# Kernel tuning notes

Measured on AMD Instinct MI355X. Metric: run time of the kernel, lower is better.

The kernel has to match this reference:

```python
import jax, jax.numpy as jnp
import numpy as np

B, S, H = 4, 1024, 1024
NH, HD = 16, 64          # heads, head_dim (NH*HD == H)
E, K, I = 8, 2, 1024     # routed experts, top_k, expert intermediate
NSH = 2                  # shared experts -> shared intermediate = NSH*I
EPS = 1e-6


def setup_inputs() -> dict:
    key = jax.random.key(0)
    ks = jax.random.split(key, 12)
    init = lambda k, shape: (jax.random.normal(k, shape, jnp.float32) * 0.02)
    return {
        "hidden_states": jax.random.normal(ks[0], (B, S, H), jnp.float32),
        "conditioning": jax.random.normal(ks[1], (B, H), jnp.float32),
        "adaLN_W": init(ks[2], (H, 6 * H)),
        "ln1_scale": jnp.ones((H,), jnp.float32),
        "ln1_bias": jnp.zeros((H,), jnp.float32),
        "ln2_scale": jnp.ones((H,), jnp.float32),
        "ln2_bias": jnp.zeros((H,), jnp.float32),
        "Wq": init(ks[3], (H, H)),
        "Wk": init(ks[4], (H, H)),
        "Wv": init(ks[5], (H, H)),
        "Wo": init(ks[6], (H, H)),
        "gate_kernel": init(ks[7], (E, H)),
        "We1": init(ks[8], (E, H, I)),
        "We2": init(ks[9], (E, I, H)),
        "Ws1": init(ks[10], (H, NSH * I)),
        "Ws2": init(ks[11], (NSH * I, H)),
    }


def _layernorm(x, scale, bias):
    m = x.mean(-1, keepdims=True)
    v = x.var(-1, keepdims=True)
    return (x - m) * jax.lax.rsqrt(v + EPS) * scale + bias


def _modulate(x, shift, scale):
    # (1 + scale) * x + shift, broadcasting [B,H] conditioning over seq dim
    return x * (1.0 + scale[:, None, :]) + shift[:, None, :]


def _attention(x, Wq, Wk, Wv, Wo):
    b, s, h = x.shape
    q = (x @ Wq).reshape(b, s, NH, HD)
    k = (x @ Wk).reshape(b, s, NH, HD)
    v = (x @ Wv).reshape(b, s, NH, HD)
    scores = jnp.einsum("bqnd,bknd->bnqk", q, k) / np.sqrt(HD).astype(np.float32)
    probs = jax.nn.softmax(scores, axis=-1)
    out = jnp.einsum("bnqk,bknd->bqnd", probs, v).reshape(b, s, h)
    return out @ Wo


def reference(hidden_states, conditioning, adaLN_W, ln1_scale, ln1_bias,
              ln2_scale, ln2_bias, Wq, Wk, Wv, Wo, gate_kernel, We1, We2,
              Ws1, Ws2):
    # adaLN modulation: SiLU -> Linear(H, 6H) -> chunk 6
    mods = jax.nn.silu(conditioning) @ adaLN_W  # [B, 6H]
    (shift_msa, scale_msa, gate_msa,
     shift_mlp, scale_mlp, gate_mlp) = jnp.split(mods, 6, axis=-1)

    normed = _modulate(_layernorm(hidden_states, ln1_scale, ln1_bias),
                       shift_msa, scale_msa)
    attn_out = _attention(normed, Wq, Wk, Wv, Wo)
    h = hidden_states + gate_msa[:, None, :] * attn_out

    normed2 = _modulate(_layernorm(h, ln2_scale, ln2_bias),
                        shift_mlp, scale_mlp)

    # --- MoE gate (DeepSeek-V2 style, greedy top-k, softmax scoring) ---
    logits = jnp.einsum("bsh,eh->bse", normed2.astype(jnp.float32),
                        gate_kernel.astype(jnp.float32))
    scores = jax.nn.softmax(logits, axis=-1)           # [B,S,E]
    topk_w, topk_idx = jax.lax.top_k(scores, K)        # [B,S,K]
    topk_w = topk_w / (topk_w.sum(-1, keepdims=True) + 1e-20)  # norm_topk_prob

    # --- dense all-expert MLPs then top-k combine (as in DiTMLPMoE) ---
    eh = jax.nn.gelu(jnp.einsum("bsh,ehi->ebsi", normed2, We1))  # [E,B,S,I]
    eo = jnp.einsum("ebsi,eih->bseh", eh, We2)                   # [B,S,E,H]
    sel = jnp.take_along_axis(eo, topk_idx[..., None], axis=2)   # [B,S,K,H]
    y = (sel * topk_w[..., None].astype(sel.dtype)).sum(axis=2)  # [B,S,H]

    # shared experts (always active)
    y = y + jax.nn.gelu(normed2 @ Ws1) @ Ws2

    return h + gate_mlp[:, None, :] * y
```

## Files before the change

### kernel.cpp

```cpp
#include <hip/hip_runtime.h>

typedef __bf16 bf16x8 __attribute__((ext_vector_type(8)));
typedef __bf16 bf16x4 __attribute__((ext_vector_type(4)));
typedef float  f32x4  __attribute__((ext_vector_type(4)));

__device__ inline float wred_sum(float v){
  #pragma unroll
  for (int d = 1; d < 64; d <<= 1) v += __shfl_xor(v, d, 64);
  return v;
}

__device__ inline float gelu_t(float x){
  const float c0 = 0.7978845608028654f;
  float t = tanhf(c0 * (x + 0.044715f * x * x * x));
  return 0.5f * x * (1.0f + t);
}

__device__ __forceinline__ void gload_lds16(const __bf16* g, __bf16* l){
  __builtin_amdgcn_global_load_lds((const __attribute__((address_space(1))) void*)g,
                                   (__attribute__((address_space(3))) void*)l, 16, 0, 0);
}

__global__ __launch_bounds__(256)
void transpose_all(const float* __restrict__ Wq, const float* __restrict__ Wk,
                   const float* __restrict__ Wv, const float* __restrict__ Wo,
                   const float* __restrict__ Ws1, const float* __restrict__ Ws2,
                   const float* __restrict__ We1, const float* __restrict__ We2,
                   __bf16* __restrict__ qkvT, __bf16* __restrict__ WoT,
                   __bf16* __restrict__ Ws1T, __bf16* __restrict__ Ws2T,
                   __bf16* __restrict__ We1T, __bf16* __restrict__ We2T){
  int z = blockIdx.z;
  const float* src; long ss; __bf16* dst; long ds;
  const long M1 = 1024 * 1024;
  if (z < 3)      { src = (z == 0 ? Wq : z == 1 ? Wk : Wv); ss = 1024; dst = qkvT + (long)z * M1; ds = 1024; }
  else if (z == 3){ src = Wo; ss = 1024; dst = WoT; ds = 1024; }
  else if (z < 6) { int ch = z - 4; src = Ws1 + ch * 1024; ss = 2048; dst = Ws1T + (long)ch * M1; ds = 1024; }
  else if (z < 8) { int rh = z - 6; src = Ws2 + (long)rh * M1; ss = 1024; dst = Ws2T + rh * 1024; ds = 2048; }
  else if (z < 16){ int e = z - 8;  src = We1 + (long)e * M1; ss = 1024; dst = We1T + (long)e * M1; ds = 1024; }
  else            { int e = z - 16; src = We2 + (long)e * M1; ss = 1024; dst = We2T + (long)e * M1; ds = 1024; }
  __shared__ float t[32][33];
  int r0 = blockIdx.y * 32, c0 = blockIdx.x * 32;
  int tid = threadIdx.x;
  int tr = tid >> 3, tc = (tid & 7) * 4;
  float4 vv = *(const float4*)&src[(long)(r0 + tr) * ss + c0 + tc];
  t[tr][tc + 0] = vv.x; t[tr][tc + 1] = vv.y; t[tr][tc + 2] = vv.z; t[tr][tc + 3] = vv.w;
  __syncthreads();
  int oc = tid >> 3, orr = (tid & 7) * 4;
  bf16x4 o4;
  #pragma unroll
  for (int i = 0; i < 4; i++) o4[i] = (__bf16)t[orr + i][oc];
  *(bf16x4*)&dst[(long)(c0 + oc) * ds + r0 + orr] = o4;
}

__global__ __launch_bounds__(256)
void adaln_k(const float* __restrict__ cond, const float* __restrict__ W, float* __restrict__ mods){
  int col = blockIdx.x * 256 + threadIdx.x;
  int kc  = blockIdx.y;
  __shared__ float sc[4][256];
  for (int i = threadIdx.x; i < 1024; i += 256){
    int b = i >> 8, r = i & 255;
    float x = cond[b * 1024 + kc * 256 + r];
    sc[b][r] = x / (1.f + expf(-x));
  }
  __syncthreads();
  float a0 = 0.f, a1 = 0.f, a2 = 0.f, a3 = 0.f;
  #pragma unroll 4
  for (int i = 0; i < 256; i++){
    float wv = W[(long)(kc * 256 + i) * 6144 + col];
    a0 += sc[0][i] * wv; a1 += sc[1][i] * wv;
    a2 += sc[2][i] * wv; a3 += sc[3][i] * wv;
  }
  atomicAdd(&mods[0 * 6144 + col], a0);
  atomicAdd(&mods[1 * 6144 + col], a1);
  atomicAdd(&mods[2 * 6144 + col], a2);
  atomicAdd(&mods[3 * 6144 + col], a3);
}

__global__ __launch_bounds__(256)
void ln_mod(const float* __restrict__ x, const float* __restrict__ sc, const float* __restrict__ bi,
            const float* __restrict__ mods, int shift_off, int scale_off, __bf16* __restrict__ out){
  int row = blockIdx.x, tid = threadIdx.x, b = row >> 10;
  float4 xv = *(const float4*)&x[(long)row * 1024 + tid * 4];
  float s  = xv.x + xv.y + xv.z + xv.w;
  float s2 = xv.x * xv.x + xv.y * xv.y + xv.z * xv.z + xv.w * xv.w;
  s = wred_sum(s); s2 = wred_sum(s2);
  __shared__ float ssum[4], ssum2[4];
  int w = tid >> 6;
  if ((tid & 63) == 0){ ssum[w] = s; ssum2[w] = s2; }
  __syncthreads();
  s = ssum[0] + ssum[1] + ssum[2] + ssum[3];
  s2 = ssum2[0] + ssum2[1] + ssum2[2] + ssum2[3];
  float mean = s * (1.f / 1024.f);
  float var  = s2 * (1.f / 1024.f) - mean * mean;
  float inv  = rsqrtf(var + 1e-6f);
  const float xa[4] = {xv.x, xv.y, xv.z, xv.w};
  #pragma unroll
  for (int i = 0; i < 4; i++){
    int c = tid * 4 + i;
    float nv = (xa[i] - mean) * inv * sc[c] + bi[c];
    nv = nv * (1.f + mods[b * 6144 + scale_off + c]) + mods[b * 6144 + shift_off + c];
    out[(long)row * 1024 + c] = (__bf16)nv;
  }
}

__global__ __launch_bounds__(256)
void gate_k(const float* __restrict__ h, const float* __restrict__ ln2s, const float* __restrict__ ln2b,
            const float* __restrict__ mods, const float* __restrict__ gw,
            int* __restrict__ eidx, float* __restrict__ wpair, __bf16* __restrict__ n2o){
  __shared__ float gws[8192];
  int tid = threadIdx.x;
  #pragma unroll
  for (int i = 0; i < 8; i++){
    int idx = tid + i * 256;
    *(float4*)&gws[idx * 4] = *(const float4*)&gw[idx * 4];
  }
  __syncthreads();
  int wv = tid >> 6, lane = tid & 63;
  int tok = blockIdx.x * 4 + wv;
  int b = tok >> 10;
  float4 xv[4]; float s = 0.f, s2 = 0.f;
  #pragma unroll
  for (int ch = 0; ch < 4; ch++){
    float4 v = *(const float4*)&h[(long)tok * 1024 + ch * 256 + lane * 4];
    xv[ch] = v;
    s  += v.x + v.y + v.z + v.w;
    s2 += v.x * v.x + v.y * v.y + v.z * v.z + v.w * v.w;
  }
  s = wred_sum(s); s2 = wred_sum(s2);
  float mean = s * (1.f / 1024.f);
  float var  = s2 * (1.f / 1024.f) - mean * mean;
  float inv  = rsqrtf(var + 1e-6f);
  float lg[8];
  #pragma unroll
  for (int e = 0; e < 8; e++) lg[e] = 0.f;
  #pragma unroll
  for (int ch = 0; ch < 4; ch++){
    int c = ch * 256 + lane * 4;
    float4 s4  = *(const float4*)&ln2s[c];
    float4 b4  = *(const float4*)&ln2b[c];
    float4 sc4 = *(const float4*)&mods[b * 6144 + 4096 + c];
    float4 sh4 = *(const float4*)&mods[b * 6144 + 3072 + c];
    float v0 = ((xv[ch].x - mean) * inv * s4.x + b4.x) * (1.f + sc4.x) + sh4.x;
    float v1 = ((xv[ch].y - mean) * inv * s4.y + b4.y) * (1.f + sc4.y) + sh4.y;
    float v2 = ((xv[ch].z - mean) * inv * s4.z + b4.z) * (1.f + sc4.z) + sh4.z;
    float v3 = ((xv[ch].w - mean) * inv * s4.w + b4.w) * (1.f + sc4.w) + sh4.w;
    *(bf16x4*)&n2o[(long)tok * 1024 + c] = (bf16x4){(__bf16)v0, (__bf16)v1, (__bf16)v2, (__bf16)v3};
    #pragma unroll
    for (int e = 0; e < 8; e++){
      float4 g4 = *(const float4*)&gws[e * 1024 + c];
      lg[e] += v0 * g4.x + v1 * g4.y + v2 * g4.z + v3 * g4.w;
    }
  }
  #pragma unroll
  for (int e = 0; e < 8; e++) lg[e] = wred_sum(lg[e]);
  if (lane == 0){
    float mx = lg[0];
    #pragma unroll
    for (int e = 1; e < 8; e++) mx = fmaxf(mx, lg[e]);
    float p[8], ss = 0.f;
    #pragma unroll
    for (int e = 0; e < 8; e++){ p[e] = expf(lg[e] - mx); ss += p[e]; }
    #pragma unroll
    for (int e = 0; e < 8; e++) p[e] /= ss;
    int i0 = 0; float b0 = p[0];
    #pragma unroll
    for (int e = 1; e < 8; e++) if (p[e] > b0){ b0 = p[e]; i0 = e; }
    int i1 = -1; float b1 = -1.f;
    #pragma unroll
    for (int e = 0; e < 8; e++) if (e != i0 && p[e] > b1){ b1 = p[e]; i1 = e; }
    float dn = b0 + b1 + 1e-20f;
    eidx[tok * 2]     = i0; wpair[tok * 2]     = b0 / dn;
    eidx[tok * 2 + 1] = i1; wpair[tok * 2 + 1] = b1 / dn;
  }
}

__global__ __launch_bounds__(256)
void build_k(const int* __restrict__ eidx, int* __restrict__ counts, int* __restrict__ lists){
  int e = blockIdx.x;
  int tid = threadIdx.x, wv = tid >> 6, lane = tid & 63;
  __shared__ int base;
  __shared__ int woff[4];
  if (tid == 0) base = 0;
  __syncthreads();
  for (int it = 0; it < 32; ++it){
    int i = it * 256 + tid;
    bool m = (eidx[i] == e);
    unsigned long long bal = __ballot(m);
    int prefix = __popcll(bal & ((1ull << lane) - 1ull));
    if (lane == 0) woff[wv] = __popcll(bal);
    __syncthreads();
    int off = base;
    #pragma unroll
    for (int k = 0; k < 4; k++) if (k < wv) off += woff[k];
    if (m) lists[e * 4096 + off + prefix] = i;
    __syncthreads();
    if (tid == 0) base += woff[0] + woff[1] + woff[2] + woff[3];
    __syncthreads();
  }
  if (tid == 0) counts[e] = base;
}

__global__ __launch_bounds__(256)
void attn_k(const __bf16* __restrict__ qkv, __bf16* __restrict__ og){
  int p = blockIdx.x + blockIdx.y * 8;
  int qblk = (p >> 3) & 7;
  int bh   = (p & 7) + ((p >> 6) << 3);
  int bb = bh >> 4, hn = bh & 15;
  int q0 = qblk * 128;
  long tokbase = (long)bb * 1024;
  int hd0 = hn * 64;
  int tid = threadIdx.x; int w = tid >> 6; int lane = tid & 63;

  __shared__ __bf16 Ks[64][76];
  __shared__ __bf16 Vt[64][76];
  __shared__ __bf16 Ps[4][32][76];

  const float QS = 0.125f * 1.44269504088896f;
  bf16x8 qf[2][2];
  #pragma unroll
  for (int sub = 0; sub < 2; sub++){
    long qrow = tokbase + q0 + sub * 64 + w * 16 + (lane & 15);
    qf[sub][0] = *(const bf16x8*)&qkv[qrow * 3072 + hd0 + (lane >> 4) * 8];
    qf[sub][1] = *(const bf16x8*)&qkv[qrow * 3072 + hd0 + 32 + (lane >> 4) * 8];
    #pragma unroll
    for (int i = 0; i < 8; i++){
      qf[sub][0][i] = (__bf16)((float)qf[sub][0][i] * QS);
      qf[sub][1][i] = (__bf16)((float)qf[sub][1][i] * QS);
    }
  }

  __bf16 one_b = (__bf16)1.0f;
  bf16x8 one8 = (bf16x8){one_b, one_b, one_b, one_b, one_b, one_b, one_b, one_b};

  float m_r[2][4];
  f32x4 oa[2][4];
  f32x4 lacc[2];
  #pragma unroll
  for (int sub = 0; sub < 2; sub++){
    lacc[sub] = (f32x4){0.f, 0.f, 0.f, 0.f};
    #pragma unroll
    for (int r = 0; r < 4; r++) m_r[sub][r] = -1e30f;
    #pragma unroll
    for (int hb = 0; hb < 4; hb++) oa[sub][hb] = (f32x4){0.f, 0.f, 0.f, 0.f};
  }

  int dcol = tid & 63, rblk = tid >> 6;
  for (int t = 0; t < 16; t++){
    long kvbase = tokbase + t * 64;
    #pragma unroll
    for (int pp = 0; pp < 2; pp++){
      int r = (tid >> 3) + pp * 32;
      int c = (tid & 7) * 8;
      *(bf16x8*)&Ks[r][c] = *(const bf16x8*)&qkv[(kvbase + r) * 3072 + 1024 + hd0 + c];
    }
    bf16x8 col0, col1;
    #pragma unroll
    for (int i = 0; i < 8; i++)
      col0[i] = qkv[(kvbase + rblk * 16 + i) * 3072 + 2048 + hd0 + dcol];
    #pragma unroll
    for (int i = 0; i < 8; i++)
      col1[i] = qkv[(kvbase + rblk * 16 + 8 + i) * 3072 + 2048 + hd0 + dcol];
    *(bf16x8*)&Vt[dcol][rblk * 16]     = col0;
    *(bf16x8*)&Vt[dcol][rblk * 16 + 8] = col1;
    __syncthreads();

    #pragma unroll
    for (int sub = 0; sub < 2; sub++){
      f32x4 sf[4];
      #pragma unroll
      for (int cb = 0; cb < 4; cb++){
        bf16x8 kf0 = *(const bf16x8*)&Ks[cb * 16 + (lane & 15)][(lane >> 4) * 8];
        bf16x8 kf1 = *(const bf16x8*)&Ks[cb * 16 + (lane & 15)][32 + (lane >> 4) * 8];
        f32x4 sacc = (f32x4){0.f, 0.f, 0.f, 0.f};
        sacc = __builtin_amdgcn_mfma_f32_16x16x32_bf16(qf[sub][0], kf0, sacc, 0, 0, 0);
        sacc = __builtin_amdgcn_mfma_f32_16x16x32_bf16(qf[sub][1], kf1, sacc, 0, 0, 0);
        sf[cb] = sacc;
      }
      float mxr[4]; float dmax = -1e30f;
      #pragma unroll
      for (int r = 0; r < 4; r++){
        float mx = fmaxf(fmaxf(sf[0][r], sf[1][r]), fmaxf(sf[2][r], sf[3][r]));
        #pragma unroll
        for (int d = 1; d < 16; d <<= 1) mx = fmaxf(mx, __shfl_xor(mx, d, 64));
        mxr[r] = mx;
        dmax = fmaxf(dmax, mx - m_r[sub][r]);
      }
      if (!__all(dmax <= 8.f)){
        #pragma unroll
        for (int r = 0; r < 4; r++){
          float mn = fmaxf(m_r[sub][r], mxr[r]);
          float fr = __builtin_amdgcn_exp2f(m_r[sub][r] - mn);
          m_r[sub][r] = mn;
          lacc[sub][r] *= fr;
          #pragma unroll
          for (int hb = 0; hb < 4; hb++) oa[sub][hb][r] *= fr;
        }
      }
      #pragma unroll
      for (int cb = 0; cb < 4; cb++)
        #pragma unroll
        for (int r = 0; r < 4; r++)
          Ps[w][sub * 16 + (lane >> 4) * 4 + r][cb * 16 + (lane & 15)] =
            (__bf16)__builtin_amdgcn_exp2f(sf[cb][r] - m_r[sub][r]);
    }
    bf16x8 pf[2][2];
    #pragma unroll
    for (int sub = 0; sub < 2; sub++){
      pf[sub][0] = *(const bf16x8*)&Ps[w][sub * 16 + (lane & 15)][(lane >> 4) * 8];
      pf[sub][1] = *(const bf16x8*)&Ps[w][sub * 16 + (lane & 15)][32 + (lane >> 4) * 8];
      lacc[sub] = __builtin_amdgcn_mfma_f32_16x16x32_bf16(pf[sub][0], one8, lacc[sub], 0, 0, 0);
      lacc[sub] = __builtin_amdgcn_mfma_f32_16x16x32_bf16(pf[sub][1], one8, lacc[sub], 0, 0, 0);
    }
    #pragma unroll
    for (int hb = 0; hb < 4; hb++){
      bf16x8 vf0 = *(const bf16x8*)&Vt[hb * 16 + (lane & 15)][(lane >> 4) * 8];
      bf16x8 vf1 = *(const bf16x8*)&Vt[hb * 16 + (lane & 15)][32 + (lane >> 4) * 8];
      #pragma unroll
      for (int sub = 0; sub < 2; sub++){
        oa[sub][hb] = __builtin_amdgcn_mfma_f32_16x16x32_bf16(pf[sub][0], vf0, oa[sub][hb], 0, 0, 0);
        oa[sub][hb] = __builtin_amdgcn_mfma_f32_16x16x32_bf16(pf[sub][1], vf1, oa[sub][hb], 0, 0, 0);
      }
    }
    __syncthreads();
  }
  #pragma unroll
  for (int sub = 0; sub < 2; sub++)
    #pragma unroll
    for (int hb = 0; hb < 4; hb++)
      #pragma unroll
      for (int r = 0; r < 4; r++){
        long row = tokbase + q0 + sub * 64 + w * 16 + (lane >> 4) * 4 + r;
        float val = oa[sub][hb][r] / lacc[sub][r];
        og[row * 1024 + hd0 + hb * 16 + (lane & 15)] = (__bf16)val;
      }
}

template<int EPI, int GMODE>
__global__ __launch_bounds__(256)
void gemm_k(const __bf16* __restrict__ A, int lda,
            const __bf16* __restrict__ Bt, int K, long bstride,
            const int* __restrict__ lists, const int* __restrict__ counts,
            __bf16* __restrict__ outb, int ldo,
            float* __restrict__ outf,
            const float* __restrict__ resid,
            const float* __restrict__ mods, int mod_off,
            const float* __restrict__ wpair,
            const float* __restrict__ addin){
  int e = blockIdx.z;
  int cnt = 1 << 30;
  const int* list = nullptr;
  if (GMODE){
    cnt = counts[e];
    if ((int)blockIdx.y * 128 >= cnt) return;
    list = lists + e * 4096;
    Bt += (long)e * bstride;
  }
  int row0 = blockIdx.y * 128;
  int n0 = blockIdx.x * 128;
  int tid = threadIdx.x;
  int lane = tid & 63, w = tid >> 6;
  int wr = (w >> 1) * 64, wc = (w & 1) * 64;

  __shared__ __bf16 As[2 * 128 * 64];
  __shared__ __bf16 Bs[2 * 128 * 64];

  f32x4 acc[4][4];
  #pragma unroll
  for (int m = 0; m < 4; m++)
    #pragma unroll
    for (int n = 0; n < 4; n++) acc[m][n] = (f32x4){0.f, 0.f, 0.f, 0.f};

  long aoff[4]; const __bf16* bptr[4];
  #pragma unroll
  for (int j = 0; j < 4; j++){
    int r = w * 32 + j * 8 + (lane >> 3);
    int scb = (lane & 7) ^ (r & 7);
    int gr = row0 + r;
    int srcr;
    if (GMODE == 0) srcr = gr;
    else if (gr < cnt){ int pv = list[gr]; srcr = (GMODE == 1) ? (pv >> 1) : pv; }
    else { int pv = list[0]; srcr = (GMODE == 1) ? (pv >> 1) : pv; }
    aoff[j] = (long)srcr * lda + scb * 8;
    bptr[j] = Bt + (long)(n0 + r) * K + scb * 8;
  }
  const int nk = K / 64;
  #pragma unroll
  for (int j = 0; j < 4; j++){
    gload_lds16(A + aoff[j], &As[(w * 32 + j * 8) * 64]);
    gload_lds16(bptr[j],     &Bs[(w * 32 + j * 8) * 64]);
  }
  __syncthreads();
  int cur = 0;
  for (int kt = 0; kt < nk; ++kt){
    int nxt = cur ^ 1;
    if (kt + 1 < nk){
      int k0 = (kt + 1) * 64;
      #pragma unroll
      for (int j = 0; j < 4; j++){
        gload_lds16(A + aoff[j] + k0, &As[nxt * 8192 + (w * 32 + j * 8) * 64]);
        gload_lds16(bptr[j] + k0,     &Bs[nxt * 8192 + (w * 32 + j * 8) * 64]);
      }
    }
    #pragma unroll
    for (int ks = 0; ks < 2; ++ks){
      bf16x8 af[4], bfr[4];
      #pragma unroll
      for (int m = 0; m < 4; m++){
        int r = wr + m * 16 + (lane & 15);
        int blk = (ks * 4 + (lane >> 4)) ^ (r & 7);
        af[m] = *(const bf16x8*)&As[cur * 8192 + r * 64 + blk * 8];
      }
      #pragma unroll
      for (int n = 0; n < 4; n++){
        int r = wc + n * 16 + (lane & 15);
        int blk = (ks * 4 + (lane >> 4)) ^ (r & 7);
        bfr[n] = *(const bf16x8*)&Bs[cur * 8192 + r * 64 + blk * 8];
      }
      #pragma unroll
      for (int m = 0; m < 4; m++)
        #pragma unroll
        for (int n = 0; n < 4; n++)
          acc[m][n] = __builtin_amdgcn_mfma_f32_16x16x32_bf16(af[m], bfr[n], acc[m][n], 0, 0, 0);
    }
    __syncthreads();
    cur = nxt;
  }
  #pragma unroll
  for (int m = 0; m < 4; m++){
    #pragma unroll
    for (int r = 0; r < 4; r++){
      int rl = wr + m * 16 + (lane >> 4) * 4 + r;
      int grow = row0 + rl;
      if (GMODE && grow >= cnt) continue;
      #pragma unroll
      for (int n = 0; n < 4; n++){
        int col = n0 + wc + n * 16 + (lane & 15);
        float v = acc[m][n][r];
        if (EPI == 0){
          outb[(long)grow * ldo + col] = (__bf16)v;
        } else if (EPI == 1){
          int dst = (GMODE == 1) ? list[grow] : grow;
          outb[(long)dst * ldo + col] = (__bf16)gelu_t(v);
        } else if (EPI == 2){
          int b = grow >> 10;
          outf[(long)grow * 1024 + col] = resid[(long)grow * 1024 + col] + mods[b * 6144 + mod_off + col] * v;
        } else if (EPI == 4){
          int pv = list[grow];
          atomicAdd(&outf[(long)(pv >> 1) * 1024 + col], wpair[pv] * v);
        } else if (EPI == 5){
          int b = grow >> 10;
          outf[(long)grow * 1024 + col] = resid[(long)grow * 1024 + col]
              + mods[b * 6144 + mod_off + col] * (v + addin[(long)grow * 1024 + col]);
        }
      }
    }
  }
}

extern "C" void kernel_launch(void* const* d_in, const int* in_sizes, int n_in,
                              void* d_out, int out_size, void* d_ws, size_t ws_size,
                              hipStream_t stream){
  const float* hidden = (const float*)d_in[0];
  const float* cond   = (const float*)d_in[1];
  const float* adaW   = (const float*)d_in[2];
  const float* ln1s   = (const float*)d_in[3];
  const float* ln1b   = (const float*)d_in[4];
  const float* ln2s   = (const float*)d_in[5];
  const float* ln2b   = (const float*)d_in[6];
  const float* Wq     = (const float*)d_in[7];
  const float* Wk     = (const float*)d_in[8];
  const float* Wv     = (const float*)d_in[9];
  const float* Wo     = (const float*)d_in[10];
  const float* gatek  = (const float*)d_in[11];
  const float* We1    = (const float*)d_in[12];
  const float* We2    = (const float*)d_in[13];
  const float* Ws1    = (const float*)d_in[14];
  const float* Ws2    = (const float*)d_in[15];
  float* out = (float*)d_out;

  const size_t MB = 1024 * 1024;
  char* W = (char*)d_ws;
  size_t off = 0;
  auto take = [&](size_t b) -> void* {
    void* p = W + off;
    off += (b + 255) & ~((size_t)255);
    return p;
  };
  float*  mods   = (float*) take(4 * 6144 * sizeof(float));
  float*  yb     = (float*) take(16 * MB);
  __bf16* qkvT   = (__bf16*)take(6 * MB);
  __bf16* WoT    = (__bf16*)take(2 * MB);
  __bf16* Ws1T   = (__bf16*)take(4 * MB);
  __bf16* Ws2T   = (__bf16*)take(4 * MB);
  __bf16* We1T   = (__bf16*)take(16 * MB);
  __bf16* We2T   = (__bf16*)take(16 * MB);
  __bf16* n1     = (__bf16*)take(8 * MB);
  __bf16* ab     = (__bf16*)take(8 * MB);
  __bf16* qkv    = (__bf16*)take(24 * MB);
  float*  hb     = (float*) take(16 * MB);
  __bf16* n2     = (__bf16*)take(8 * MB);
  int*    counts = (int*)   take(256);
  int*    lists  = (int*)   take(8 * 4096 * 4);
  float*  wpair  = (float*) take(8192 * 4);
  int*    eidx   = (int*)   take(8192 * 4);
  __bf16* EH = n1;
  __bf16* SH = qkv;

  dim3 blk(256);

  hipMemsetAsync(mods, 0, 4 * 6144 * sizeof(float) + 16 * MB, stream);

  transpose_all<<<dim3(32, 32, 24), blk, 0, stream>>>(Wq, Wk, Wv, Wo, Ws1, Ws2, We1, We2,
                                                      qkvT, WoT, Ws1T, Ws2T, We1T, We2T);

  adaln_k<<<dim3(24, 4), blk, 0, stream>>>(cond, adaW, mods);

  ln_mod<<<4096, blk, 0, stream>>>(hidden, ln1s, ln1b, mods, 0, 1024, n1);

  gemm_k<0, 0><<<dim3(24, 32, 1), blk, 0, stream>>>(n1, 1024, qkvT, 1024, 0, nullptr, nullptr, qkv, 3072, nullptr, nullptr, nullptr, 0, nullptr, nullptr);

  attn_k<<<dim3(8, 64, 1), blk, 0, stream>>>(qkv, ab);

  gemm_k<2, 0><<<dim3(8, 32, 1), blk, 0, stream>>>(ab, 1024, WoT, 1024, 0, nullptr, nullptr, nullptr, 0, hb, hidden, mods, 2048, nullptr, nullptr);

  gate_k<<<1024, blk, 0, stream>>>(hb, ln2s, ln2b, mods, gatek, eidx, wpair, n2);
  build_k<<<8, blk, 0, stream>>>(eidx, counts, lists);

  gemm_k<1, 1><<<dim3(8, 32, 8), blk, 0, stream>>>(n2, 1024, We1T, 1024, 1048576, lists, counts, EH, 1024, nullptr, nullptr, nullptr, 0, nullptr, nullptr);
  gemm_k<4, 2><<<dim3(8, 32, 8), blk, 0, stream>>>(EH, 1024, We2T, 1024, 1048576, lists, counts, nullptr, 0, yb, nullptr, nullptr, 0, wpair, nullptr);

  gemm_k<1, 0><<<dim3(16, 32, 1), blk, 0, stream>>>(n2, 1024, Ws1T, 1024, 0, nullptr, nullptr, SH, 2048, nullptr, nullptr, nullptr, 0, nullptr, nullptr);
  gemm_k<5, 0><<<dim3(8, 32, 1), blk, 0, stream>>>(SH, 2048, Ws2T, 2048, 0, nullptr, nullptr, nullptr, 0, out, hb, mods, 5120, nullptr, yb);

  (void)in_sizes; (void)n_in; (void)out_size; (void)ws_size;
}
```

Baseline: 560.9 us.

## Merge routed and shared up-projection GEMMs, replace atomics with bf16 scatter buffer

The GEMM kernel moves to 512 threads with 8 waves each holding a 64x32 sub-tile, and drops the LDS double buffering in favour of a single-stage load-then-compute loop. The routed expert up-projection and the shared-expert up-projection now run in one launch, selected by the z index. The down-projection writes weighted per-pair outputs to a bf16 buffer instead of doing float atomicAdds, and the final shared GEMM epilogue sums the two pair rows. This removes the atomics, the 16 MB memset and one launch, at the cost of losing load/compute overlap inside the GEMM and rounding the expert outputs to bf16.

```diff
diff --git a/kernel.cpp b/kernel.cpp
--- a/kernel.cpp
+++ b/kernel.cpp
@@ -336,94 +336,101 @@
 }
 
 template<int EPI, int GMODE>
-__global__ __launch_bounds__(256)
+__global__ __launch_bounds__(512)
 void gemm_k(const __bf16* __restrict__ A, int lda,
             const __bf16* __restrict__ Bt, int K, long bstride,
+            const __bf16* __restrict__ Bt2,
             const int* __restrict__ lists, const int* __restrict__ counts,
             __bf16* __restrict__ outb, int ldo,
+            __bf16* __restrict__ outb2, int ldo2,
             float* __restrict__ outf,
             const float* __restrict__ resid,
             const float* __restrict__ mods, int mod_off,
             const float* __restrict__ wpair,
-            const float* __restrict__ addin){
-  int e = blockIdx.z;
+            const __bf16* __restrict__ eo){
+  int z = blockIdx.z;
   int cnt = 1 << 30;
   const int* list = nullptr;
-  if (GMODE){
-    cnt = counts[e];
+  const __bf16* B = Bt;
+  __bf16* OB = outb; int LDO = ldo;
+  bool shp = false;
+  if (GMODE == 2){
+    cnt = counts[z];
     if ((int)blockIdx.y * 128 >= cnt) return;
-    list = lists + e * 4096;
-    Bt += (long)e * bstride;
+    list = lists + z * 4096;
+    B = Bt + (long)z * bstride;
+  } else if (GMODE == 3){
+    if (z < 8){
+      cnt = counts[z];
+      if ((int)blockIdx.y * 128 >= cnt) return;
+      list = lists + z * 4096;
+      B = Bt + (long)z * bstride;
+    } else {
+      shp = true;
+      B = Bt2 + (long)(z - 8) * bstride;
+      OB = outb2 + (long)(z - 8) * 1024; LDO = ldo2;
+    }
   }
   int row0 = blockIdx.y * 128;
   int n0 = blockIdx.x * 128;
   int tid = threadIdx.x;
   int lane = tid & 63, w = tid >> 6;
-  int wr = (w >> 1) * 64, wc = (w & 1) * 64;
-
-  __shared__ __bf16 As[2 * 128 * 64];
-  __shared__ __bf16 Bs[2 * 128 * 64];
-
-  f32x4 acc[4][4];
+  int wr = (w >> 2) * 64, wc = (w & 3) * 32;
+
+  __shared__ __bf16 As[128 * 64];
+  __shared__ __bf16 Bs[128 * 64];
+
+  f32x4 acc[4][2];
   #pragma unroll
   for (int m = 0; m < 4; m++)
     #pragma unroll
-    for (int n = 0; n < 4; n++) acc[m][n] = (f32x4){0.f, 0.f, 0.f, 0.f};
-
-  long aoff[4]; const __bf16* bptr[4];
-  #pragma unroll
-  for (int j = 0; j < 4; j++){
-    int r = w * 32 + j * 8 + (lane >> 3);
+    for (int n = 0; n < 2; n++) acc[m][n] = (f32x4){0.f, 0.f, 0.f, 0.f};
+
+  long aoff[2]; const __bf16* bptr[2];
+  #pragma unroll
+  for (int j = 0; j < 2; j++){
+    int r = j * 64 + w * 8 + (lane >> 3);
     int scb = (lane & 7) ^ (r & 7);
     int gr = row0 + r;
     int srcr;
-    if (GMODE == 0) srcr = gr;
-    else if (gr < cnt){ int pv = list[gr]; srcr = (GMODE == 1) ? (pv >> 1) : pv; }
-    else { int pv = list[0]; srcr = (GMODE == 1) ? (pv >> 1) : pv; }
+    bool routed = (GMODE == 2) || (GMODE == 3 && !shp);
+    if (!routed) srcr = gr;
+    else if (gr < cnt){ int pv = list[gr]; srcr = (GMODE == 3) ? (pv >> 1) : pv; }
+    else { int pv = list[0]; srcr = (GMODE == 3) ? (pv >> 1) : pv; }
     aoff[j] = (long)srcr * lda + scb * 8;
-    bptr[j] = Bt + (long)(n0 + r) * K + scb * 8;
+    bptr[j] = B + (long)(n0 + r) * K + scb * 8;
   }
   const int nk = K / 64;
-  #pragma unroll
-  for (int j = 0; j < 4; j++){
-    gload_lds16(A + aoff[j], &As[(w * 32 + j * 8) * 64]);
-    gload_lds16(bptr[j],     &Bs[(w * 32 + j * 8) * 64]);
-  }
-  __syncthreads();
-  int cur = 0;
   for (int kt = 0; kt < nk; ++kt){
-    int nxt = cur ^ 1;
-    if (kt + 1 < nk){
-      int k0 = (kt + 1) * 64;
-      #pragma unroll
-      for (int j = 0; j < 4; j++){
-        gload_lds16(A + aoff[j] + k0, &As[nxt * 8192 + (w * 32 + j * 8) * 64]);
-        gload_lds16(bptr[j] + k0,     &Bs[nxt * 8192 + (w * 32 + j * 8) * 64]);
-      }
-    }
+    int k0 = kt * 64;
+    #pragma unroll
+    for (int j = 0; j < 2; j++){
+      gload_lds16(A + aoff[j] + k0, &As[(j * 64 + w * 8) * 64]);
+      gload_lds16(bptr[j] + k0,     &Bs[(j * 64 + w * 8) * 64]);
+    }
+    __syncthreads();
     #pragma unroll
     for (int ks = 0; ks < 2; ++ks){
-      bf16x8 af[4], bfr[4];
+      bf16x8 af[4], bfr[2];
       #pragma unroll
       for (int m = 0; m < 4; m++){
         int r = wr + m * 16 + (lane & 15);
         int blk = (ks * 4 + (lane >> 4)) ^ (r & 7);
-        af[m] = *(const bf16x8*)&As[cur * 8192 + r * 64 + blk * 8];
-      }
-      #pragma unroll
-      for (int n = 0; n < 4; n++){
+        af[m] = *(const bf16x8*)&As[r * 64 + blk * 8];
+      }
+      #pragma unroll
+      for (int n = 0; n < 2; n++){
         int r = wc + n * 16 + (lane & 15);
         int blk = (ks * 4 + (lane >> 4)) ^ (r & 7);
-        bfr[n] = *(const bf16x8*)&Bs[cur * 8192 + r * 64 + blk * 8];
+        bfr[n] = *(const bf16x8*)&Bs[r * 64 + blk * 8];
       }
       #pragma unroll
       for (int m = 0; m < 4; m++)
         #pragma unroll
-        for (int n = 0; n < 4; n++)
+        for (int n = 0; n < 2; n++)
           acc[m][n] = __builtin_amdgcn_mfma_f32_16x16x32_bf16(af[m], bfr[n], acc[m][n], 0, 0, 0);
     }
     __syncthreads();
-    cur = nxt;
   }
   #pragma unroll
   for (int m = 0; m < 4; m++){
@@ -431,26 +438,27 @@
     for (int r = 0; r < 4; r++){
       int rl = wr + m * 16 + (lane >> 4) * 4 + r;
       int grow = row0 + rl;
-      if (GMODE && grow >= cnt) continue;
-      #pragma unroll
-      for (int n = 0; n < 4; n++){
+      if ((GMODE == 2 || (GMODE == 3 && !shp)) && grow >= cnt) continue;
+      #pragma unroll
+      for (int n = 0; n < 2; n++){
         int col = n0 + wc + n * 16 + (lane & 15);
         float v = acc[m][n][r];
         if (EPI == 0){
-          outb[(long)grow * ldo + col] = (__bf16)v;
+          OB[(long)grow * LDO + col] = (__bf16)v;
         } else if (EPI == 1){
-          int dst = (GMODE == 1) ? list[grow] : grow;
-          outb[(long)dst * ldo + col] = (__bf16)gelu_t(v);
+          int dst = (GMODE == 3 && !shp) ? list[grow] : grow;
+          OB[(long)dst * LDO + col] = (__bf16)gelu_t(v);
         } else if (EPI == 2){
           int b = grow >> 10;
           outf[(long)grow * 1024 + col] = resid[(long)grow * 1024 + col] + mods[b * 6144 + mod_off + col] * v;
-        } else if (EPI == 4){
-          int pv = list[grow];
-          atomicAdd(&outf[(long)(pv >> 1) * 1024 + col], wpair[pv] * v);
         } else if (EPI == 5){
           int b = grow >> 10;
+          float add = (float)eo[(long)(grow * 2) * 1024 + col] + (float)eo[(long)(grow * 2 + 1) * 1024 + col];
           outf[(long)grow * 1024 + col] = resid[(long)grow * 1024 + col]
-              + mods[b * 6144 + mod_off + col] * (v + addin[(long)grow * 1024 + col]);
+              + mods[b * 6144 + mod_off + col] * (v + add);
+        } else if (EPI == 6){
+          int pv = list[grow];
+          OB[(long)pv * LDO + col] = (__bf16)(wpair[pv] * v);
         }
       }
     }
@@ -487,7 +495,7 @@
     return p;
   };
   float*  mods   = (float*) take(4 * 6144 * sizeof(float));
-  float*  yb     = (float*) take(16 * MB);
+  __bf16* EO     = (__bf16*)take(16 * MB);
   __bf16* qkvT   = (__bf16*)take(6 * MB);
   __bf16* WoT    = (__bf16*)take(2 * MB);
   __bf16* Ws1T   = (__bf16*)take(4 * MB);
@@ -506,9 +514,9 @@
   __bf16* EH = n1;
   __bf16* SH = qkv;
 
-  dim3 blk(256);
-
-  hipMemsetAsync(mods, 0, 4 * 6144 * sizeof(float) + 16 * MB, stream);
+  dim3 blk(256), blk5(512);
+
+  hipMemsetAsync(mods, 0, 4 * 6144 * sizeof(float), stream);
 
   transpose_all<<<dim3(32, 32, 24), blk, 0, stream>>>(Wq, Wk, Wv, Wo, Ws1, Ws2, We1, We2,
                                                       qkvT, WoT, Ws1T, Ws2T, We1T, We2T);
@@ -517,20 +525,25 @@
 
   ln_mod<<<4096, blk, 0, stream>>>(hidden, ln1s, ln1b, mods, 0, 1024, n1);
 
-  gemm_k<0, 0><<<dim3(24, 32, 1), blk, 0, stream>>>(n1, 1024, qkvT, 1024, 0, nullptr, nullptr, qkv, 3072, nullptr, nullptr, nullptr, 0, nullptr, nullptr);
+  gemm_k<0, 0><<<dim3(24, 32, 1), blk5, 0, stream>>>(n1, 1024, qkvT, 1024, 0, nullptr, nullptr, nullptr,
+      qkv, 3072, nullptr, 0, nullptr, nullptr, nullptr, 0, nullptr, nullptr);
 
   attn_k<<<dim3(8, 64, 1), blk, 0, stream>>>(qkv, ab);
 
-  gemm_k<2, 0><<<dim3(8, 32, 1), blk, 0, stream>>>(ab, 1024, WoT, 1024, 0, nullptr, nullptr, nullptr, 0, hb, hidden, mods, 2048, nullptr, nullptr);
+  gemm_k<2, 0><<<dim3(8, 32, 1), blk5, 0, stream>>>(ab, 1024, WoT, 1024, 0, nullptr, nullptr, nullptr,
+      nullptr, 0, nullptr, 0, hb, hidden, mods, 2048, nullptr, nullptr);
 
   gate_k<<<1024, blk, 0, stream>>>(hb, ln2s, ln2b, mods, gatek, eidx, wpair, n2);
   build_k<<<8, blk, 0, stream>>>(eidx, counts, lists);
 
-  gemm_k<1, 1><<<dim3(8, 32, 8), blk, 0, stream>>>(n2, 1024, We1T, 1024, 1048576, lists, counts, EH, 1024, nullptr, nullptr, nullptr, 0, nullptr, nullptr);
-  gemm_k<4, 2><<<dim3(8, 32, 8), blk, 0, stream>>>(EH, 1024, We2T, 1024, 1048576, lists, counts, nullptr, 0, yb, nullptr, nullptr, 0, wpair, nullptr);
-
-  gemm_k<1, 0><<<dim3(16, 32, 1), blk, 0, stream>>>(n2, 1024, Ws1T, 1024, 0, nullptr, nullptr, SH, 2048, nullptr, nullptr, nullptr, 0, nullptr, nullptr);
-  gemm_k<5, 0><<<dim3(8, 32, 1), blk, 0, stream>>>(SH, 2048, Ws2T, 2048, 0, nullptr, nullptr, nullptr, 0, out, hb, mods, 5120, nullptr, yb);
+  gemm_k<1, 3><<<dim3(8, 32, 10), blk5, 0, stream>>>(n2, 1024, We1T, 1024, 1048576, Ws1T, lists, counts,
+      EH, 1024, SH, 2048, nullptr, nullptr, nullptr, 0, nullptr, nullptr);
+
+  gemm_k<6, 2><<<dim3(8, 32, 8), blk5, 0, stream>>>(EH, 1024, We2T, 1024, 1048576, nullptr, lists, counts,
+      EO, 1024, nullptr, 0, nullptr, nullptr, nullptr, 0, wpair, nullptr);
+
+  gemm_k<5, 0><<<dim3(8, 32, 1), blk5, 0, stream>>>(SH, 2048, Ws2T, 2048, 0, nullptr, nullptr, nullptr,
+      nullptr, 0, nullptr, 0, out, hb, mods, 5120, nullptr, EO);
 
   (void)in_sizes; (void)n_in; (void)out_size; (void)ws_size;
 }
```

Measured after the change: 484.3 us. 13.6% less time.
